# Performance work log

Measured on AMD Instinct MI355X. Metric: run time of the kernel, lower is better.

The kernel has to match this reference:

```python
import jax, jax.numpy as jnp
import numpy as np

EMBED_DIM = 1024
NUM_HEADS = 16
HEAD_DIM = EMBED_DIM // NUM_HEADS
B, N = 4, 2048


def setup_inputs() -> dict:
    key = jax.random.key(0)
    k = jax.random.split(key, 5)
    scale = 1.0 / np.sqrt(EMBED_DIM)
    return {
        "x": jax.random.normal(k[0], (B, N, EMBED_DIM), dtype=jnp.float32),
        # torch nn.Linear convention: y = x @ W.T + b, W shape [out, in]
        "qkv_w": jax.random.uniform(k[1], (3 * EMBED_DIM, EMBED_DIM), jnp.float32, -scale, scale),
        "qkv_b": jax.random.uniform(k[2], (3 * EMBED_DIM,), jnp.float32, -scale, scale),
        "out_w": jax.random.uniform(k[3], (EMBED_DIM, EMBED_DIM), jnp.float32, -scale, scale),
        "out_b": jax.random.uniform(k[4], (EMBED_DIM,), jnp.float32, -scale, scale),
    }


def reference(x, qkv_w, qkv_b, out_w, out_b):
    b, n, e = x.shape
    qkv = x @ qkv_w.T + qkv_b                      # [B,N,3E]
    qkv = qkv.reshape(b, n, 3, NUM_HEADS, HEAD_DIM)
    qkv = jnp.transpose(qkv, (2, 0, 3, 1, 4))      # [3,B,H,N,D]
    q, k, v = qkv[0], qkv[1], qkv[2]
    scores = jnp.einsum("bhqd,bhkd->bhqk", q, k) / np.sqrt(HEAD_DIM)
    weights = jax.nn.softmax(scores, axis=-1)
    attn = jnp.einsum("bhqk,bhkd->bhqd", weights, v)  # [B,H,N,D]
    attn = jnp.transpose(attn, (0, 2, 1, 3)).reshape(b, n, e)
    return attn @ out_w.T + out_b
```

## Files before the change

kernel.cpp:

```cpp
#include <hip/hip_runtime.h>
#include <hip/hip_bf16.h>

#define EMBED 1024
#define NHEADS 16
#define HDIM 64
#define BATCH 4
#define SEQ 2048
#define MROWS (BATCH*SEQ)
#define QKVN (3*EMBED)
#define KDIM 1024

typedef __bf16 bf16;
typedef __bf16 bf16x4 __attribute__((ext_vector_type(4)));
typedef __bf16 bf16x8 __attribute__((ext_vector_type(8)));
typedef float f32x4 __attribute__((ext_vector_type(4)));
typedef float f32x16 __attribute__((ext_vector_type(16)));

#define QSCALE 0.18033688011112042f

#define SWB(B) ((B) ^ ((((B) >> 9) & 1) << 4) ^ ((((B) >> 7) & 1) << 5))

#define NX (MROWS*EMBED/4)
#define NQ (QKVN*KDIM/4)
#define NO (EMBED*KDIM/4)
__global__ void cvt_all(const float* __restrict__ x, const float* __restrict__ qw,
                        const float* __restrict__ ow,
                        bf16* __restrict__ xb, bf16* __restrict__ qwb, bf16* __restrict__ owb) {
    int i = blockIdx.x * blockDim.x + threadIdx.x;
    const float* src; bf16* dst; int j;
    if (i < NX)            { src = x;  dst = xb;  j = i; }
    else if (i < NX + NQ)  { src = qw; dst = qwb; j = i - NX; }
    else if (i < NX+NQ+NO) { src = ow; dst = owb; j = i - NX - NQ; }
    else return;
    float4 f = ((const float4*)src)[j];
    bf16x4 o;
    o[0] = (bf16)f.x; o[1] = (bf16)f.y; o[2] = (bf16)f.z; o[3] = (bf16)f.w;
    *((bf16x4*)dst + j) = o;
}

__launch_bounds__(256)
__global__ void gemm_qkv(const bf16* __restrict__ A, const bf16* __restrict__ B,
                         const float* __restrict__ bias,
                         bf16* __restrict__ Qb, bf16* __restrict__ Kb, bf16* __restrict__ Vt)
{
    __shared__ __align__(16) char ldsmem[32768];
    char* A0 = ldsmem;
    char* B0 = ldsmem + 8192;
    char* A1 = ldsmem + 16384;
    char* B1 = ldsmem + 24576;
    char* bnc = ldsmem;

    const int tid = threadIdx.x;
    const int l = tid & 63, w = tid >> 6;
    const int wr = w >> 1, wc = w & 1;
    const int tM = blockIdx.y * 128, tN = blockIdx.x * 128;

    f32x4 acc[4][4] = {};
    const bf16* Abase = A + (size_t)tM * KDIM;
    const bf16* Bbase = B + (size_t)tN * KDIM;

#define GSTAGE(AL, BL, KOFF)                                                             \
    {                                                                                    \
        int koff_ = (KOFF) < KDIM ? (KOFF) : 0;                                          \
        _Pragma("unroll")                                                                \
        for (int t = 0; t < 2; ++t) {                                                    \
            int idx = t * 256 + tid;                                                     \
            int row = idx >> 2;                                                          \
            int kc = (idx & 3) * 8;                                                      \
            __builtin_amdgcn_global_load_lds(                                            \
                (const __attribute__((address_space(1))) void*)(Abase + (size_t)row * KDIM + koff_ + kc), \
                (__attribute__((address_space(3))) void*)((AL) + idx * 16), 16, 0, 0);   \
            __builtin_amdgcn_global_load_lds(                                            \
                (const __attribute__((address_space(1))) void*)(Bbase + (size_t)row * KDIM + koff_ + kc), \
                (__attribute__((address_space(3))) void*)((BL) + idx * 16), 16, 0, 0);   \
        }                                                                                \
    }

#define GBODY(AL, BL, KNEXT)                                                             \
    {                                                                                    \
        bf16x8 a[4], b[4];                                                               \
        _Pragma("unroll")                                                                \
        for (int i = 0; i < 4; ++i)                                                      \
            a[i] = *(const bf16x8*)((AL) + ((wr * 64 + i * 16 + (l & 15)) * 32 + (l >> 4) * 8) * 2); \
        _Pragma("unroll")                                                                \
        for (int j = 0; j < 4; ++j)                                                      \
            b[j] = *(const bf16x8*)((BL) + ((wc * 64 + j * 16 + (l & 15)) * 32 + (l >> 4) * 8) * 2); \
        asm volatile("s_waitcnt lgkmcnt(0)" ::: "memory");                               \
        __builtin_amdgcn_sched_barrier(0);                                               \
        __builtin_amdgcn_s_barrier();                                                    \
        __builtin_amdgcn_sched_barrier(0);                                               \
        GSTAGE(AL, BL, KNEXT)                                                            \
        _Pragma("unroll")                                                                \
        for (int i = 0; i < 4; ++i)                                                      \
            _Pragma("unroll")                                                            \
            for (int j = 0; j < 4; ++j)                                                  \
                acc[i][j] = __builtin_amdgcn_mfma_f32_16x16x32_bf16(a[i], b[j], acc[i][j], 0, 0, 0); \
        asm volatile("s_waitcnt vmcnt(4)" ::: "memory");                                 \
        __builtin_amdgcn_sched_barrier(0);                                               \
        __builtin_amdgcn_s_barrier();                                                    \
        __builtin_amdgcn_sched_barrier(0);                                               \
    }

    GSTAGE(A0, B0, 0)
    GSTAGE(A1, B1, 32)
    asm volatile("s_waitcnt vmcnt(4)" ::: "memory");
    __builtin_amdgcn_sched_barrier(0);
    __builtin_amdgcn_s_barrier();
    __builtin_amdgcn_sched_barrier(0);

    for (int k0 = 0; k0 < KDIM; k0 += 64) {
        GBODY(A0, B0, k0 + 64)
        GBODY(A1, B1, k0 + 96)
    }
#undef GBODY
#undef GSTAGE

    const int which = tN >> 10;
    const int bidx  = tM >> 11;
    const int hd0   = (tN & 1023) >> 6;
    const int t32base = (tM & 2047) >> 5;
    bf16* dstbase = (which == 0) ? Qb : (which == 1) ? Kb : Vt;
    const float scale = (which == 0) ? QSCALE : 1.0f;

    float bj[4];
    #pragma unroll
    for (int j = 0; j < 4; ++j)
        bj[j] = bias[tN + wc * 64 + j * 16 + (l & 15)];

    #pragma unroll
    for (int pass = 0; pass < 2; ++pass) {
        __syncthreads();
        #pragma unroll
        for (int ii = 0; ii < 2; ++ii) {
            const int i = pass * 2 + ii;
            #pragma unroll
            for (int j = 0; j < 4; ++j) {
                const int d = (wc * 64 + j * 16 + (l & 15)) & 63;
                #pragma unroll
                for (int r = 0; r < 4; ++r) {
                    const int nsl = wr * 64 + i * 16 + (l >> 4) * 4 + r;
                    float v = acc[i][j][r] + bj[j];
                    int off;
                    if (which == 2) {
                        int dblk = d >> 5;
                        int rem16 = nsl & 15;
                        int c = (nsl >> 4) & 1;
                        int fj = (rem16 & 3) | ((rem16 & 8) >> 1);
                        int fhi = (rem16 >> 2) & 1;
                        int lane = (d & 31) | (fhi << 5);
                        off = (dblk * 2 + c) * 512 + lane * 8 + fj;
                    } else {
                        int kk = d >> 4, fhi = (d >> 3) & 1, fj = d & 7;
                        int lane = (nsl & 31) | (fhi << 5);
                        off = kk * 512 + lane * 8 + fj;
                    }
                    *(bf16*)(bnc + (wc * 2 + wr) * 4096 + SWB(off * 2)) = (bf16)(v * scale);
                }
            }
        }
        __syncthreads();
        const int chunk = tid >> 6;
        size_t gbase = ((size_t)(bidx * NHEADS + hd0 + (chunk >> 1)) * 64
                        + t32base + 2 * (chunk & 1) + pass) * 2048;
        #pragma unroll
        for (int s = 0; s < 4; ++s) {
            int boff = SWB((s * 512 + (tid & 63) * 8) * 2);
            *(bf16x8*)(dstbase + gbase + (size_t)(s * 512 + (tid & 63) * 8)) =
                *(const bf16x8*)(bnc + chunk * 4096 + boff);
        }
    }
}

__launch_bounds__(256)
__global__ void gemm_out(const bf16* __restrict__ A, const bf16* __restrict__ B,
                         const float* __restrict__ bias, float* __restrict__ outF)
{
    __shared__ __align__(16) char lds64[24576];
    char* A0 = lds64;
    char* B0 = lds64 + 4096;
    char* A1 = lds64 + 12288;
    char* B1 = lds64 + 16384;
    const int tid = threadIdx.x;
    const int l = tid & 63, w = tid >> 6;
    const int tM = blockIdx.y * 64, tN = blockIdx.x * 128;

    f32x4 acc[4][2] = {};
    const bf16* Abase = A + (size_t)tM * KDIM;
    const bf16* Bbase = B + (size_t)tN * KDIM;

#define OSTAGE(AL, BL, KOFF)                                                             \
    {                                                                                    \
        int koff_ = (KOFF) < KDIM ? (KOFF) : 0;                                          \
        {                                                                                \
            int row = tid >> 2;                                                          \
            int kc = (tid & 3) * 8;                                                      \
            __builtin_amdgcn_global_load_lds(                                            \
                (const __attribute__((address_space(1))) void*)(Abase + (size_t)row * KDIM + koff_ + kc), \
                (__attribute__((address_space(3))) void*)((AL) + tid * 16), 16, 0, 0);   \
        }                                                                                \
        _Pragma("unroll")                                                                \
        for (int t = 0; t < 2; ++t) {                                                    \
            int idx = t * 256 + tid;                                                     \
            int row = idx >> 2;                                                          \
            int kc = (idx & 3) * 8;                                                      \
            __builtin_amdgcn_global_load_lds(                                            \
                (const __attribute__((address_space(1))) void*)(Bbase + (size_t)row * KDIM + koff_ + kc), \
                (__attribute__((address_space(3))) void*)((BL) + idx * 16), 16, 0, 0);   \
        }                                                                                \
    }

#define OBODY(AL, BL, KNEXT)                                                             \
    {                                                                                    \
        bf16x8 a[4], b[2];                                                               \
        _Pragma("unroll")                                                                \
        for (int i = 0; i < 4; ++i)                                                      \
            a[i] = *(const bf16x8*)((AL) + ((i * 16 + (l & 15)) * 32 + (l >> 4) * 8) * 2); \
        _Pragma("unroll")                                                                \
        for (int j = 0; j < 2; ++j)                                                      \
            b[j] = *(const bf16x8*)((BL) + ((w * 32 + j * 16 + (l & 15)) * 32 + (l >> 4) * 8) * 2); \
        asm volatile("s_waitcnt lgkmcnt(0)" ::: "memory");                               \
        __builtin_amdgcn_sched_barrier(0);                                               \
        __builtin_amdgcn_s_barrier();                                                    \
        __builtin_amdgcn_sched_barrier(0);                                               \
        OSTAGE(AL, BL, KNEXT)                                                            \
        _Pragma("unroll")                                                                \
        for (int i = 0; i < 4; ++i)                                                      \
            _Pragma("unroll")                                                            \
            for (int j = 0; j < 2; ++j)                                                  \
                acc[i][j] = __builtin_amdgcn_mfma_f32_16x16x32_bf16(a[i], b[j], acc[i][j], 0, 0, 0); \
        asm volatile("s_waitcnt vmcnt(3)" ::: "memory");                                 \
        __builtin_amdgcn_sched_barrier(0);                                               \
        __builtin_amdgcn_s_barrier();                                                    \
        __builtin_amdgcn_sched_barrier(0);                                               \
    }

    OSTAGE(A0, B0, 0)
    OSTAGE(A1, B1, 32)
    asm volatile("s_waitcnt vmcnt(3)" ::: "memory");
    __builtin_amdgcn_sched_barrier(0);
    __builtin_amdgcn_s_barrier();
    __builtin_amdgcn_sched_barrier(0);

    for (int k0 = 0; k0 < KDIM; k0 += 64) {
        OBODY(A0, B0, k0 + 64)
        OBODY(A1, B1, k0 + 96)
    }
#undef OBODY
#undef OSTAGE

    #pragma unroll
    for (int i = 0; i < 4; ++i) {
        #pragma unroll
        for (int j = 0; j < 2; ++j) {
            int n = tN + w * 32 + j * 16 + (l & 15);
            float bv = bias[n];
            #pragma unroll
            for (int r = 0; r < 4; ++r) {
                int m = tM + i * 16 + (l >> 4) * 4 + r;
                outF[(size_t)m * EMBED + n] = acc[i][j][r] + bv;
            }
        }
    }
}

static __device__ __forceinline__ unsigned cvt_pk(float lo, float hi) {
    unsigned r;
    asm("v_cvt_pk_bf16_f32 %0, %1, %2" : "=v"(r) : "v"(lo), "v"(hi));
    return r;
}

__launch_bounds__(256, 4)
__global__ void attn_kernel(const bf16* __restrict__ Qb, const bf16* __restrict__ Kb,
                            const bf16* __restrict__ Vt, bf16* __restrict__ AO)
{
    __shared__ bf16 kv[2][2][2048];
    const int tid = threadIdx.x, l = tid & 63, w = tid >> 6;
    const int lo5 = l & 31, hi = l >> 5;
    int bid = blockIdx.x;
    int swz = (bid & 7) * 128 + (bid >> 3);
    const int bh = swz >> 4;
    const int qt = swz & 15;

    const bf16* QFh = Qb + (size_t)bh * (64 * 2048);
    const bf16* Ksrc = Kb + (size_t)bh * (64 * 2048) + w * 512 + l * 8;
    const bf16* Vsrc = Vt + (size_t)bh * (64 * 2048) + w * 512 + l * 8;

    const int qtile = qt * 4 + w;
    const bf16* qbase = QFh + (size_t)qtile * 2048 + (size_t)l * 8;
    bf16x8 qf[4];
    #pragma unroll
    for (int kk = 0; kk < 4; ++kk)
        qf[kk] = *(const bf16x8*)(qbase + kk * 512);

    f32x16 O0 = {}, O1 = {};
    float lsum = 0.f;

#define STAGE(BUF)                                                                       \
    {                                                                                    \
        __builtin_amdgcn_global_load_lds(                                                \
            (const __attribute__((address_space(1))) void*)Ksrc,                         \
            (__attribute__((address_space(3))) void*)&kv[BUF][0][w * 512], 16, 0, 0);    \
        __builtin_amdgcn_global_load_lds(                                                \
            (const __attribute__((address_space(1))) void*)Vsrc,                         \
            (__attribute__((address_space(3))) void*)&kv[BUF][1][w * 512], 16, 0, 0);    \
        Ksrc += 2048; Vsrc += 2048;                                                      \
    }

    STAGE(0)
    __syncthreads();

#define ATTN_BODY(B)                                                                     \
    {                                                                                    \
        STAGE(B ^ 1)                                                                     \
        bf16x8 kK0 = *(const bf16x8*)&kv[B][0][0 * 512 + l * 8];                         \
        bf16x8 kK1 = *(const bf16x8*)&kv[B][0][1 * 512 + l * 8];                         \
        bf16x8 kK2 = *(const bf16x8*)&kv[B][0][2 * 512 + l * 8];                         \
        bf16x8 kK3 = *(const bf16x8*)&kv[B][0][3 * 512 + l * 8];                         \
        bf16x8 vf00 = *(const bf16x8*)&kv[B][1][0 * 512 + l * 8];                        \
        bf16x8 vf01 = *(const bf16x8*)&kv[B][1][1 * 512 + l * 8];                        \
        bf16x8 vf10 = *(const bf16x8*)&kv[B][1][2 * 512 + l * 8];                        \
        bf16x8 vf11 = *(const bf16x8*)&kv[B][1][3 * 512 + l * 8];                        \
        f32x16 S = {};                                                                   \
        __builtin_amdgcn_s_setprio(1);                                                   \
        S = __builtin_amdgcn_mfma_f32_32x32x16_bf16(kK0, qf[0], S, 0, 0, 0);             \
        S = __builtin_amdgcn_mfma_f32_32x32x16_bf16(kK1, qf[1], S, 0, 0, 0);             \
        S = __builtin_amdgcn_mfma_f32_32x32x16_bf16(kK2, qf[2], S, 0, 0, 0);             \
        S = __builtin_amdgcn_mfma_f32_32x32x16_bf16(kK3, qf[3], S, 0, 0, 0);             \
        __builtin_amdgcn_s_setprio(0);                                                   \
        float p[16];                                                                     \
        _Pragma("unroll")                                                                \
        for (int r = 0; r < 16; ++r)                                                     \
            p[r] = __builtin_amdgcn_exp2f(S[r]);                                         \
        float s0 = (p[0] + p[1]) + (p[2] + p[3]);                                        \
        float s1 = (p[4] + p[5]) + (p[6] + p[7]);                                        \
        float s2 = (p[8] + p[9]) + (p[10] + p[11]);                                      \
        float s3 = (p[12] + p[13]) + (p[14] + p[15]);                                    \
        lsum += (s0 + s1) + (s2 + s3);                                                   \
        union { unsigned u[4]; bf16x8 v; } pk0, pk1;                                     \
        pk0.u[0] = cvt_pk(p[0], p[1]);   pk0.u[1] = cvt_pk(p[2], p[3]);                  \
        pk0.u[2] = cvt_pk(p[4], p[5]);   pk0.u[3] = cvt_pk(p[6], p[7]);                  \
        pk1.u[0] = cvt_pk(p[8], p[9]);   pk1.u[1] = cvt_pk(p[10], p[11]);                \
        pk1.u[2] = cvt_pk(p[12], p[13]); pk1.u[3] = cvt_pk(p[14], p[15]);                \
        __builtin_amdgcn_s_setprio(1);                                                   \
        O0 = __builtin_amdgcn_mfma_f32_32x32x16_bf16(vf00, pk0.v, O0, 0, 0, 0);          \
        O0 = __builtin_amdgcn_mfma_f32_32x32x16_bf16(vf01, pk1.v, O0, 0, 0, 0);          \
        O1 = __builtin_amdgcn_mfma_f32_32x32x16_bf16(vf10, pk0.v, O1, 0, 0, 0);          \
        O1 = __builtin_amdgcn_mfma_f32_32x32x16_bf16(vf11, pk1.v, O1, 0, 0, 0);          \
        __builtin_amdgcn_s_setprio(0);                                                   \
        __syncthreads();                                                                 \
    }

    for (int t2 = 0; t2 < 64; t2 += 2) {
        ATTN_BODY(0)
        ATTN_BODY(1)
    }
#undef ATTN_BODY
#undef STAGE

    lsum += __shfl_xor(lsum, 32);
    float linv = 1.0f / lsum;

    const int b = bh >> 4, hd = bh & 15;
    const int q0 = qt * 128 + w * 32;
    bf16* outp = &AO[(size_t)(b * SEQ + q0 + lo5) * EMBED + hd * HDIM];
    #pragma unroll
    for (int g = 0; g < 4; ++g) {
        bf16x4 o0, o1;
        #pragma unroll
        for (int r4 = 0; r4 < 4; ++r4) {
            o0[r4] = (bf16)(O0[g * 4 + r4] * linv);
            o1[r4] = (bf16)(O1[g * 4 + r4] * linv);
        }
        *(bf16x4*)&outp[g * 8 + hi * 4] = o0;
        *(bf16x4*)&outp[32 + g * 8 + hi * 4] = o1;
    }
}

extern "C" void kernel_launch(void* const* d_in, const int* in_sizes, int n_in,
                              void* d_out, int out_size, void* d_ws, size_t ws_size,
                              hipStream_t stream) {
    const float* x     = (const float*)d_in[0];
    const float* qkv_w = (const float*)d_in[1];
    const float* qkv_b = (const float*)d_in[2];
    const float* out_w = (const float*)d_in[3];
    const float* out_b = (const float*)d_in[4];
    float* out = (float*)d_out;

    char* ws = (char*)d_ws;
    bf16* xb  = (bf16*)(ws);
    bf16* qwb = (bf16*)(ws + 16777216);
    bf16* owb = (bf16*)(ws + 23068672);
    bf16* Qb  = (bf16*)(ws + 25165824);
    bf16* Kb  = (bf16*)(ws + 41943040);
    bf16* Vt  = (bf16*)(ws + 58720256);
    bf16* AO  = (bf16*)(ws + 75497472);

    cvt_all<<<(NX + NQ + NO + 255) / 256, 256, 0, stream>>>(x, qkv_w, out_w, xb, qwb, owb);

    gemm_qkv<<<dim3(QKVN / 128, MROWS / 128), 256, 0, stream>>>(
        xb, qwb, qkv_b, Qb, Kb, Vt);

    attn_kernel<<<BATCH * NHEADS * (SEQ / 128), 256, 0, stream>>>(Qb, Kb, Vt, AO);

    gemm_out<<<dim3(EMBED / 128, MROWS / 64), 256, 0, stream>>>(AO, owb, out_b, out);
}
```

Before: 187.0 us.

## Restructure GEMM K-loop to ping-pong double buffering with one barrier per step

The QKV and output-projection GEMM main loops used to run two barriers per K-step: they waited for LDS reads, synced, then refilled the same buffer. They now issue the global-to-LDS loads for the next buffer at the top of the step, compute on the current buffer, and sync once after a full vmcnt(0) drain. MFMA sections are also wrapped in s_setprio(1) to favour issue of the math waves. This removes one barrier per step, but the prefetch distance drops to one stage and each step waits for all outstanding loads, which may expose more memory latency.

```diff
diff --git a/kernel.cpp b/kernel.cpp
--- a/kernel.cpp
+++ b/kernel.cpp
@@ -76,43 +76,42 @@
         }                                                                                \
     }
 
-#define GBODY(AL, BL, KNEXT)                                                             \
-    {                                                                                    \
+#define TBODY(CA, CB, NA, NB, KNEXT)                                                     \
+    {                                                                                    \
+        GSTAGE(NA, NB, KNEXT)                                                            \
         bf16x8 a[4], b[4];                                                               \
         _Pragma("unroll")                                                                \
         for (int i = 0; i < 4; ++i)                                                      \
-            a[i] = *(const bf16x8*)((AL) + ((wr * 64 + i * 16 + (l & 15)) * 32 + (l >> 4) * 8) * 2); \
+            a[i] = *(const bf16x8*)((CA) + ((wr * 64 + i * 16 + (l & 15)) * 32 + (l >> 4) * 8) * 2); \
         _Pragma("unroll")                                                                \
         for (int j = 0; j < 4; ++j)                                                      \
-            b[j] = *(const bf16x8*)((BL) + ((wc * 64 + j * 16 + (l & 15)) * 32 + (l >> 4) * 8) * 2); \
+            b[j] = *(const bf16x8*)((CB) + ((wc * 64 + j * 16 + (l & 15)) * 32 + (l >> 4) * 8) * 2); \
         asm volatile("s_waitcnt lgkmcnt(0)" ::: "memory");                               \
         __builtin_amdgcn_sched_barrier(0);                                               \
-        __builtin_amdgcn_s_barrier();                                                    \
-        __builtin_amdgcn_sched_barrier(0);                                               \
-        GSTAGE(AL, BL, KNEXT)                                                            \
+        __builtin_amdgcn_s_setprio(1);                                                   \
         _Pragma("unroll")                                                                \
         for (int i = 0; i < 4; ++i)                                                      \
             _Pragma("unroll")                                                            \
             for (int j = 0; j < 4; ++j)                                                  \
                 acc[i][j] = __builtin_amdgcn_mfma_f32_16x16x32_bf16(a[i], b[j], acc[i][j], 0, 0, 0); \
-        asm volatile("s_waitcnt vmcnt(4)" ::: "memory");                                 \
+        __builtin_amdgcn_s_setprio(0);                                                   \
+        asm volatile("s_waitcnt vmcnt(0)" ::: "memory");                                 \
         __builtin_amdgcn_sched_barrier(0);                                               \
         __builtin_amdgcn_s_barrier();                                                    \
         __builtin_amdgcn_sched_barrier(0);                                               \
     }
 
     GSTAGE(A0, B0, 0)
-    GSTAGE(A1, B1, 32)
-    asm volatile("s_waitcnt vmcnt(4)" ::: "memory");
+    asm volatile("s_waitcnt vmcnt(0)" ::: "memory");
     __builtin_amdgcn_sched_barrier(0);
     __builtin_amdgcn_s_barrier();
     __builtin_amdgcn_sched_barrier(0);
 
     for (int k0 = 0; k0 < KDIM; k0 += 64) {
-        GBODY(A0, B0, k0 + 64)
-        GBODY(A1, B1, k0 + 96)
-    }
-#undef GBODY
+        TBODY(A0, B0, A1, B1, k0 + 32)
+        TBODY(A1, B1, A0, B0, k0 + 64)
+    }
+#undef TBODY
 #undef GSTAGE
 
     const int which = tN >> 10;
@@ -209,43 +208,42 @@
         }                                                                                \
     }
 
-#define OBODY(AL, BL, KNEXT)                                                             \
-    {                                                                                    \
+#define OTBODY(CA, CB, NA, NB, KNEXT)                                                    \
+    {                                                                                    \
+        OSTAGE(NA, NB, KNEXT)                                                            \
         bf16x8 a[4], b[2];                                                               \
         _Pragma("unroll")                                                                \
         for (int i = 0; i < 4; ++i)                                                      \
-            a[i] = *(const bf16x8*)((AL) + ((i * 16 + (l & 15)) * 32 + (l >> 4) * 8) * 2); \
+            a[i] = *(const bf16x8*)((CA) + ((i * 16 + (l & 15)) * 32 + (l >> 4) * 8) * 2); \
         _Pragma("unroll")                                                                \
         for (int j = 0; j < 2; ++j)                                                      \
-            b[j] = *(const bf16x8*)((BL) + ((w * 32 + j * 16 + (l & 15)) * 32 + (l >> 4) * 8) * 2); \
+            b[j] = *(const bf16x8*)((CB) + ((w * 32 + j * 16 + (l & 15)) * 32 + (l >> 4) * 8) * 2); \
         asm volatile("s_waitcnt lgkmcnt(0)" ::: "memory");                               \
         __builtin_amdgcn_sched_barrier(0);                                               \
-        __builtin_amdgcn_s_barrier();                                                    \
-        __builtin_amdgcn_sched_barrier(0);                                               \
-        OSTAGE(AL, BL, KNEXT)                                                            \
+        __builtin_amdgcn_s_setprio(1);                                                   \
         _Pragma("unroll")                                                                \
         for (int i = 0; i < 4; ++i)                                                      \
             _Pragma("unroll")                                                            \
             for (int j = 0; j < 2; ++j)                                                  \
                 acc[i][j] = __builtin_amdgcn_mfma_f32_16x16x32_bf16(a[i], b[j], acc[i][j], 0, 0, 0); \
-        asm volatile("s_waitcnt vmcnt(3)" ::: "memory");                                 \
+        __builtin_amdgcn_s_setprio(0);                                                   \
+        asm volatile("s_waitcnt vmcnt(0)" ::: "memory");                                 \
         __builtin_amdgcn_sched_barrier(0);                                               \
         __builtin_amdgcn_s_barrier();                                                    \
         __builtin_amdgcn_sched_barrier(0);                                               \
     }
 
     OSTAGE(A0, B0, 0)
-    OSTAGE(A1, B1, 32)
-    asm volatile("s_waitcnt vmcnt(3)" ::: "memory");
+    asm volatile("s_waitcnt vmcnt(0)" ::: "memory");
     __builtin_amdgcn_sched_barrier(0);
     __builtin_amdgcn_s_barrier();
     __builtin_amdgcn_sched_barrier(0);
 
     for (int k0 = 0; k0 < KDIM; k0 += 64) {
-        OBODY(A0, B0, k0 + 64)
-        OBODY(A1, B1, k0 + 96)
-    }
-#undef OBODY
+        OTBODY(A0, B0, A1, B1, k0 + 32)
+        OTBODY(A1, B1, A0, B0, k0 + 64)
+    }
+#undef OTBODY
 #undef OSTAGE
 
     #pragma unroll
```

New measurement: 186.0 us. Within noise of the previous version (-0.5%).
